# Performance work log

Measured on AMD Instinct MI355X. Metric: run time of the kernel, lower is better.

## Reference

```python
import jax, jax.numpy as jnp
import numpy as np

NUM_GRAPHS = 2048
NODES_PER_GRAPH = 256
N_NODES = NUM_GRAPHS * NODES_PER_GRAPH
N_EDGES = 2 * N_NODES
F_IN = 768
HID = 128
N_CLS = 2


def setup_inputs() -> dict:
    key = jax.random.key(0)
    ks = jax.random.split(key, 12)
    x = jax.random.normal(ks[0], (N_NODES, F_IN), dtype=jnp.float32)
    edge_index = jax.random.randint(ks[1], (2, N_EDGES), 0, N_NODES, dtype=jnp.int32)
    batch = jnp.repeat(jnp.arange(NUM_GRAPHS, dtype=jnp.int32), NODES_PER_GRAPH)
    s = 1.0 / np.sqrt(F_IN)
    sh = 1.0 / np.sqrt(HID)
    s2h = 1.0 / np.sqrt(2 * HID)
    return {
        "x": x,
        "edge_index": edge_index,
        "batch": batch,
        # SAGEConv: lin_l (aggregated neighbors, with bias) + lin_r (root, no bias)
        "W_l": jax.random.uniform(ks[2], (F_IN, HID), jnp.float32, -s, s),
        "b_l": jax.random.uniform(ks[3], (HID,), jnp.float32, -s, s),
        "W_r": jax.random.uniform(ks[4], (F_IN, HID), jnp.float32, -s, s),
        "W0": jax.random.uniform(ks[5], (F_IN, HID), jnp.float32, -s, s),
        "b0": jax.random.uniform(ks[6], (HID,), jnp.float32, -s, s),
        "W1": jax.random.uniform(ks[7], (2 * HID, HID), jnp.float32, -s2h, s2h),
        "b1": jax.random.uniform(ks[8], (HID,), jnp.float32, -s2h, s2h),
        "W2": jax.random.uniform(ks[9], (HID, N_CLS), jnp.float32, -sh, sh),
        "b2": jax.random.uniform(ks[10], (HID,), jnp.float32, -sh, sh)[:N_CLS],
    }


def reference(x, edge_index, batch, W_l, b_l, W_r, W0, b0, W1, b1, W2, b2):
    n = x.shape[0]
    src, dst = edge_index[0], edge_index[1]
    # SAGEConv with mean aggregation: gather -> segment mean -> transform
    msg_sum = jax.ops.segment_sum(x[src], dst, num_segments=n)      # [N, F]
    cnt = jax.ops.segment_sum(jnp.ones((src.shape[0],), x.dtype), dst, num_segments=n)
    agg = msg_sum / jnp.maximum(cnt, 1.0)[:, None]
    h = jax.nn.relu(agg @ W_l + b_l + x @ W_r)                       # [N, H]
    # global max pool per graph
    pooled = jax.ops.segment_max(h, batch, num_segments=NUM_GRAPHS)  # [G, H]
    # root (news) node = first node of each graph (batch is sorted)
    roots = jnp.searchsorted(batch, jnp.arange(NUM_GRAPHS, dtype=batch.dtype))
    news = jax.nn.relu(x[roots] @ W0 + b0)                           # [G, H]
    z = jax.nn.relu(jnp.concatenate([pooled, news], axis=1) @ W1 + b1)
    return jax.nn.log_softmax(z @ W2 + b2, axis=-1)                  # [G, 2]
```

## Files before the change

kernel.cpp:

```cpp
#include <hip/hip_runtime.h>

#define NGRAPH 2048
#define NPG 256
#define NNODE (NGRAPH*NPG)
#define NEDGE (2*NNODE)
#define FIN 768
#define HID 128
#define SLOTS 64
#define BK 32
#define NKT (FIN/BK)

typedef __bf16 bf16x8 __attribute__((ext_vector_type(8)));
typedef __bf16 bf16x4 __attribute__((ext_vector_type(4)));
typedef float f32x4 __attribute__((ext_vector_type(4)));

__device__ __forceinline__ float bflo(unsigned v) {
    return __uint_as_float((v & 0xffffu) << 16);
}
__device__ __forceinline__ float bfhi(unsigned v) {
    return __uint_as_float(v & 0xffff0000u);
}

__global__ __launch_bounds__(256) void k_prep(
    const float* __restrict__ Wl, const float* __restrict__ Wr,
    const float* __restrict__ W0, __bf16* __restrict__ WbT,
    int* __restrict__ deg)
{
    int idx = blockIdx.x * 256 + threadIdx.x;
    deg[idx] = 0;
    if (idx < 384 * FIN) {
        int n = idx / FIN;
        int k = idx - n * FIN;
        float v;
        if (n < HID)            v = Wl[k * HID + n];
        else if (n < 2 * HID)   v = Wr[k * HID + (n - HID)];
        else                    v = W0[k * HID + (n - 2 * HID)];
        WbT[idx] = (__bf16)v;
    }
}

template<int VMC, bool HASB, bool HASA, bool HASW>
__device__ __forceinline__ void gemm_tile(
    const char* rbuf, char* wbuf, int t, int lane, int wr, int wc,
    const float* asrc, const __bf16* WbT, int ktB, int ktA,
    f32x4& c0, f32x4& c1, f32x4& c2, f32x4& c3,
    f32x4& i0, f32x4& i1, f32x4& i2, f32x4& i3,
    int aoff0, int aoff1, f32x4 (&acc)[8][4])
{
    if constexpr (HASB) {
#pragma unroll
        for (int r = 0; r < 2; ++r) {
            int idx = r * 512 + t;
            int bn = idx >> 2, bj = idx & 3;
            int koff = (bj ^ ((bn >> 1) & 3)) << 3;
            const __bf16* g = WbT + bn * FIN + ktB * BK + koff;
            __builtin_amdgcn_global_load_lds(
                (__attribute__((address_space(1))) void*)g,
                (__attribute__((address_space(3))) void*)(wbuf + 16384 + idx * 16),
                16, 0, 0);
        }
        __builtin_amdgcn_sched_barrier(0);
    }
    if constexpr (HASA) {
        const f32x4* s4 = (const f32x4*)(asrc + ktA * BK);
        i0 = s4[0]; i1 = s4[1]; i2 = s4[2]; i3 = s4[3];
    }
    if constexpr (HASW) {
        bf16x8 h0, h1;
#pragma unroll
        for (int i = 0; i < 4; ++i) {
            h0[i]     = (__bf16)c0[i];
            h0[4 + i] = (__bf16)c1[i];
            h1[i]     = (__bf16)c2[i];
            h1[4 + i] = (__bf16)c3[i];
        }
        *(bf16x8*)(wbuf + aoff0) = h0;
        *(bf16x8*)(wbuf + aoff1) = h1;
    }
    const int kb = (lane >> 4) << 4;
    bf16x8 a[8], b[4];
#pragma unroll
    for (int m = 0; m < 8; ++m) {
        int row = wr * 128 + m * 16 + (lane & 15);
        a[m] = *(const bf16x8*)(rbuf + row * 64 + (kb ^ (((row >> 1) & 3) << 4)));
    }
#pragma unroll
    for (int n = 0; n < 4; ++n) {
        int row = wc * 64 + n * 16 + (lane & 15);
        b[n] = *(const bf16x8*)(rbuf + 16384 + row * 64 + (kb ^ (((row >> 1) & 3) << 4)));
    }
#pragma unroll
    for (int m = 0; m < 8; ++m)
#pragma unroll
        for (int n = 0; n < 4; ++n)
            acc[m][n] = __builtin_amdgcn_mfma_f32_16x16x32_bf16(
                a[m], b[n], acc[m][n], 0, 0, 0);
    if constexpr (VMC == 4) asm volatile("s_waitcnt vmcnt(4)" ::: "memory");
    else if constexpr (VMC == 0) asm volatile("s_waitcnt vmcnt(0)" ::: "memory");
    if constexpr (VMC >= 0) {
        asm volatile("s_waitcnt lgkmcnt(0)" ::: "memory");
        __builtin_amdgcn_s_barrier();
    }
}

__global__ __launch_bounds__(512, 1) void k_gemm(
    const float* __restrict__ X, const __bf16* __restrict__ WbT,
    __bf16* __restrict__ Yl, __bf16* __restrict__ Yr,
    const int* __restrict__ ei, int* __restrict__ deg, int* __restrict__ elist,
    const float* __restrict__ b0, float* __restrict__ news)
{
    __shared__ __align__(16) char sm[65536];
    const int t = threadIdx.x;
    const int lane = t & 63;
    const int w = t >> 6;

    if (blockIdx.x >= NNODE / 256) {
        const int wr = w >> 2;
        const int wc = w & 3;
        const int g0 = (blockIdx.x - NNODE / 256) * 64;

        f32x4 acc[2][2];
#pragma unroll
        for (int m = 0; m < 2; ++m)
#pragma unroll
            for (int n = 0; n < 2; ++n)
                acc[m][n] = (f32x4){0.f, 0.f, 0.f, 0.f};

        const int arow = t >> 3;
        const int ak = (t & 7) * 4;
        const float* asrc = X + (size_t)(g0 + arow) * (NPG * FIN) + ak;
        const int aoff = arow * 64 + (((ak * 2) ^ (((arow >> 1) & 3) << 4)));
        const __bf16* W0bT = WbT + (size_t)256 * FIN;

        for (int kt = 0; kt < NKT; ++kt) {
            const int k0 = kt * BK;
            __syncthreads();
            {
                f32x4 p = *(const f32x4*)(asrc + k0);
                bf16x4 h;
#pragma unroll
                for (int i = 0; i < 4; ++i) h[i] = (__bf16)p[i];
                *(bf16x4*)(sm + aoff) = h;
            }
            {
                int bn = t >> 2;
                int bj = t & 3;
                int koff = (bj ^ ((bn >> 1) & 3)) << 3;
                const __bf16* g = W0bT + bn * FIN + k0 + koff;
                __builtin_amdgcn_global_load_lds(
                    (__attribute__((address_space(1))) void*)g,
                    (__attribute__((address_space(3))) void*)(sm + 4096 + t * 16),
                    16, 0, 0);
            }
            __syncthreads();

            const int kb = (lane >> 4) << 4;
            bf16x8 a[2], b[2];
#pragma unroll
            for (int m = 0; m < 2; ++m) {
                int row = wr * 32 + m * 16 + (lane & 15);
                a[m] = *(const bf16x8*)(sm + row * 64 + (kb ^ (((row >> 1) & 3) << 4)));
            }
#pragma unroll
            for (int n = 0; n < 2; ++n) {
                int row = wc * 32 + n * 16 + (lane & 15);
                b[n] = *(const bf16x8*)(sm + 4096 + row * 64 + (kb ^ (((row >> 1) & 3) << 4)));
            }
#pragma unroll
            for (int m = 0; m < 2; ++m)
#pragma unroll
                for (int n = 0; n < 2; ++n)
                    acc[m][n] = __builtin_amdgcn_mfma_f32_16x16x32_bf16(
                        a[m], b[n], acc[m][n], 0, 0, 0);
        }

#pragma unroll
        for (int m = 0; m < 2; ++m) {
            const int rbase = wr * 32 + m * 16 + ((lane >> 4) << 2);
#pragma unroll
            for (int n = 0; n < 2; ++n) {
                const int col = wc * 32 + n * 16 + (lane & 15);
                const float bb = b0[col];
#pragma unroll
                for (int j = 0; j < 4; ++j)
                    news[(size_t)(g0 + rbase + j) * HID + col] =
                        fmaxf(acc[m][n][j] + bb, 0.f);
            }
        }
        return;
    }

    {
        int e = blockIdx.x * 512 + t;
        int src = ei[e];
        int dst = ei[NEDGE + e];
        int pos = atomicAdd(deg + dst, 1);
        if (pos < SLOTS) elist[(size_t)pos * NNODE + dst] = src;
    }
    asm volatile("s_waitcnt vmcnt(0)" ::: "memory");

    const int wr = w >> 2;
    const int wc = w & 3;
    const size_t node0 = (size_t)blockIdx.x * 256;

    f32x4 acc[8][4];
#pragma unroll
    for (int m = 0; m < 8; ++m)
#pragma unroll
        for (int n = 0; n < 4; ++n)
            acc[m][n] = (f32x4){0.f, 0.f, 0.f, 0.f};

    const int arow = t >> 1;
    const int ak = (t & 1) * 16;
    const float* asrc = X + (node0 + arow) * FIN + ak;
    const int axr = ((arow >> 1) & 3) << 4;
    const int aoff0 = arow * 64 + ((ak * 2) ^ axr);
    const int aoff1 = arow * 64 + ((ak * 2 + 16) ^ axr);

    char* buf0 = sm;
    char* buf1 = sm + 32768;
    f32x4 qa0, qa1, qa2, qa3;
    f32x4 qb0, qb1, qb2, qb3;

    {
#pragma unroll
        for (int r = 0; r < 2; ++r) {
            int idx = r * 512 + t;
            int bn = idx >> 2, bj = idx & 3;
            int koff = (bj ^ ((bn >> 1) & 3)) << 3;
            const __bf16* g = WbT + bn * FIN + 0 * BK + koff;
            __builtin_amdgcn_global_load_lds(
                (__attribute__((address_space(1))) void*)g,
                (__attribute__((address_space(3))) void*)(buf0 + 16384 + idx * 16),
                16, 0, 0);
        }
        __builtin_amdgcn_sched_barrier(0);
        {
            const f32x4* s4 = (const f32x4*)(asrc);
            qa0 = s4[0]; qa1 = s4[1]; qa2 = s4[2]; qa3 = s4[3];
        }
        {
            const f32x4* s4 = (const f32x4*)(asrc + 1 * BK);
            qb0 = s4[0]; qb1 = s4[1]; qb2 = s4[2]; qb3 = s4[3];
        }
        bf16x8 h0, h1;
#pragma unroll
        for (int i = 0; i < 4; ++i) {
            h0[i]     = (__bf16)qa0[i];
            h0[4 + i] = (__bf16)qa1[i];
            h1[i]     = (__bf16)qa2[i];
            h1[4 + i] = (__bf16)qa3[i];
        }
        *(bf16x8*)(buf0 + aoff0) = h0;
        *(bf16x8*)(buf0 + aoff1) = h1;
        asm volatile("s_waitcnt vmcnt(4)" ::: "memory");
        asm volatile("s_waitcnt lgkmcnt(0)" ::: "memory");
        __builtin_amdgcn_s_barrier();
    }

    for (int kt = 0; kt < 22; kt += 2) {
        gemm_tile<4, true, true, true>(buf0, buf1, t, lane, wr, wc, asrc, WbT,
            kt + 1, kt + 2, qb0, qb1, qb2, qb3, qa0, qa1, qa2, qa3,
            aoff0, aoff1, acc);
        gemm_tile<4, true, true, true>(buf1, buf0, t, lane, wr, wc, asrc, WbT,
            kt + 2, kt + 3, qa0, qa1, qa2, qa3, qb0, qb1, qb2, qb3,
            aoff0, aoff1, acc);
    }
    gemm_tile<0, true, false, true>(buf0, buf1, t, lane, wr, wc, asrc, WbT,
        23, 0, qb0, qb1, qb2, qb3, qa0, qa1, qa2, qa3, aoff0, aoff1, acc);
    gemm_tile<-1, false, false, false>(buf1, buf0, t, lane, wr, wc, asrc, WbT,
        0, 0, qa0, qa1, qa2, qa3, qb0, qb1, qb2, qb3, aoff0, aoff1, acc);

#pragma unroll
    for (int m = 0; m < 8; ++m) {
        const int rbase = wr * 128 + m * 16 + ((lane >> 4) << 2);
#pragma unroll
        for (int n = 0; n < 4; ++n) {
            const int col = wc * 64 + n * 16 + (lane & 15);
            __bf16* dst = (col < HID) ? Yl : Yr;
            const int c = col & (HID - 1);
#pragma unroll
            for (int j = 0; j < 4; ++j)
                dst[(node0 + rbase + j) * HID + c] = (__bf16)acc[m][n][j];
        }
    }
}

__global__ __launch_bounds__(512) void k_fused(
    const int* __restrict__ deg, const int* __restrict__ elist,
    const __bf16* __restrict__ Yl, const __bf16* __restrict__ Yr,
    const float* __restrict__ bl, const float* __restrict__ news,
    const float* __restrict__ W1, const float* __restrict__ b1,
    const float* __restrict__ W2, const float* __restrict__ b2,
    float* __restrict__ out)
{
    __shared__ int   sdeg[NPG];
    __shared__ int   sel[4 * NPG];
    __shared__ float red[8 * HID];
    __shared__ float cat[2 * HID];
    __shared__ float zs[HID];

    const int g = blockIdx.x;
    const int t = threadIdx.x;
    const size_t gbase = (size_t)g * NPG;

    if (t < NPG) sdeg[t] = deg[gbase + t];
#pragma unroll
    for (int r = 0; r < 2; ++r) {
        int idx = r * 512 + t;
        sel[idx] = elist[(size_t)(idx >> 8) * NNODE + gbase + (idx & 255)];
    }
    __syncthreads();

    const int l = t & 63;
    const int sub = t >> 6;
    const int half = l >> 5;
    const int lj = l & 31;
    const int d4 = lj * 4;
    const float4 blv = *(const float4*)(bl + d4);
    const uint2* yl2 = (const uint2*)Yl;
    const uint2* yr2 = (const uint2*)Yr;

    float m0 = -3.0e38f, m1 = -3.0e38f, m2 = -3.0e38f, m3 = -3.0e38f;

    for (int k4 = 0; k4 < 8; ++k4) {
        const int nA = sub + 8 * (4 * k4 + half);
        const int nB = sub + 8 * (4 * k4 + 2 + half);
        const int dgA = sdeg[nA], dgB = sdeg[nB];
        int sA[4], sB[4];
#pragma unroll
        for (int j = 0; j < 4; ++j) {
            int cA = sel[j * NPG + nA];
            int cB = sel[j * NPG + nB];
            sA[j] = (j < dgA) ? cA : 0;
            sB[j] = (j < dgB) ? cB : 0;
        }
        uint2 vA[4], vB[4];
#pragma unroll
        for (int j = 0; j < 4; ++j) {
            vA[j] = yl2[(size_t)sA[j] * 32 + lj];
            vB[j] = yl2[(size_t)sB[j] * 32 + lj];
        }
        const uint2 yA = yr2[(gbase + nA) * 32 + lj];
        const uint2 yB = yr2[(gbase + nB) * 32 + lj];

        float s0A = 0.f, s1A = 0.f, s2A = 0.f, s3A = 0.f;
        float s0B = 0.f, s1B = 0.f, s2B = 0.f, s3B = 0.f;
#pragma unroll
        for (int j = 0; j < 4; ++j) {
            const float mA = (j < dgA) ? 1.f : 0.f;
            const float mB = (j < dgB) ? 1.f : 0.f;
            s0A = fmaf(mA, bflo(vA[j].x), s0A);
            s1A = fmaf(mA, bfhi(vA[j].x), s1A);
            s2A = fmaf(mA, bflo(vA[j].y), s2A);
            s3A = fmaf(mA, bfhi(vA[j].y), s3A);
            s0B = fmaf(mB, bflo(vB[j].x), s0B);
            s1B = fmaf(mB, bfhi(vB[j].x), s1B);
            s2B = fmaf(mB, bflo(vB[j].y), s2B);
            s3B = fmaf(mB, bfhi(vB[j].y), s3B);
        }
        int mx = dgA > dgB ? dgA : dgB;
        mx = max(mx, __shfl_xor(mx, 32));
        mx = mx < SLOTS ? mx : SLOTS;
        for (int j = 4; j < mx; ++j) {
            int cA = elist[(size_t)j * NNODE + gbase + nA];
            int cB = elist[(size_t)j * NNODE + gbase + nB];
            int eA = (j < dgA) ? cA : 0;
            int eB = (j < dgB) ? cB : 0;
            uint2 wA = yl2[(size_t)eA * 32 + lj];
            uint2 wB = yl2[(size_t)eB * 32 + lj];
            const float mA = (j < dgA) ? 1.f : 0.f;
            const float mB = (j < dgB) ? 1.f : 0.f;
            s0A = fmaf(mA, bflo(wA.x), s0A);
            s1A = fmaf(mA, bfhi(wA.x), s1A);
            s2A = fmaf(mA, bflo(wA.y), s2A);
            s3A = fmaf(mA, bfhi(wA.y), s3A);
            s0B = fmaf(mB, bflo(wB.x), s0B);
            s1B = fmaf(mB, bfhi(wB.x), s1B);
            s2B = fmaf(mB, bflo(wB.y), s2B);
            s3B = fmaf(mB, bfhi(wB.y), s3B);
        }
        const float invA = 1.f / fmaxf((float)dgA, 1.f);
        const float invB = 1.f / fmaxf((float)dgB, 1.f);
        float h0 = fmaf(s0A, invA, blv.x) + bflo(yA.x);
        float h1 = fmaf(s1A, invA, blv.y) + bfhi(yA.x);
        float h2 = fmaf(s2A, invA, blv.z) + bflo(yA.y);
        float h3 = fmaf(s3A, invA, blv.w) + bfhi(yA.y);
        m0 = fmaxf(m0, fmaxf(h0, 0.f));
        m1 = fmaxf(m1, fmaxf(h1, 0.f));
        m2 = fmaxf(m2, fmaxf(h2, 0.f));
        m3 = fmaxf(m3, fmaxf(h3, 0.f));
        h0 = fmaf(s0B, invB, blv.x) + bflo(yB.x);
        h1 = fmaf(s1B, invB, blv.y) + bfhi(yB.x);
        h2 = fmaf(s2B, invB, blv.z) + bflo(yB.y);
        h3 = fmaf(s3B, invB, blv.w) + bfhi(yB.y);
        m0 = fmaxf(m0, fmaxf(h0, 0.f));
        m1 = fmaxf(m1, fmaxf(h1, 0.f));
        m2 = fmaxf(m2, fmaxf(h2, 0.f));
        m3 = fmaxf(m3, fmaxf(h3, 0.f));
    }
    m0 = fmaxf(m0, __shfl_xor(m0, 32));
    m1 = fmaxf(m1, __shfl_xor(m1, 32));
    m2 = fmaxf(m2, __shfl_xor(m2, 32));
    m3 = fmaxf(m3, __shfl_xor(m3, 32));
    if (half == 0) {
        float4 mv = {m0, m1, m2, m3};
        *(float4*)(red + sub * HID + d4) = mv;
    }
    __syncthreads();

    if (t < HID) {
        float v = red[t];
#pragma unroll
        for (int s = 1; s < 8; ++s) v = fmaxf(v, red[s * HID + t]);
        cat[t] = v;
        cat[HID + t] = news[(size_t)g * HID + t];
    }
    __syncthreads();

    if (t < HID) {
        float a0 = 0.f, a1 = 0.f, a2 = 0.f, a3 = 0.f;
        for (int k = 0; k < 2 * HID; k += 4) {
            a0 = fmaf(cat[k + 0], W1[(k + 0) * HID + t], a0);
            a1 = fmaf(cat[k + 1], W1[(k + 1) * HID + t], a1);
            a2 = fmaf(cat[k + 2], W1[(k + 2) * HID + t], a2);
            a3 = fmaf(cat[k + 3], W1[(k + 3) * HID + t], a3);
        }
        zs[t] = fmaxf((a0 + a1) + (a2 + a3) + b1[t], 0.f);
    }
    __syncthreads();

    if (t < 64) {
        float z0 = zs[t * 2], z1 = zs[t * 2 + 1];
        float p0 = fmaf(z0, W2[t * 4 + 0], z1 * W2[t * 4 + 2]);
        float p1 = fmaf(z0, W2[t * 4 + 1], z1 * W2[t * 4 + 3]);
#pragma unroll
        for (int off = 32; off; off >>= 1) {
            p0 += __shfl_down(p0, off);
            p1 += __shfl_down(p1, off);
        }
        if (t == 0) {
            float l0 = p0 + b2[0], l1 = p1 + b2[1];
            float mx = fmaxf(l0, l1);
            float lse = mx + logf(expf(l0 - mx) + expf(l1 - mx));
            out[(size_t)g * 2 + 0] = l0 - lse;
            out[(size_t)g * 2 + 1] = l1 - lse;
        }
    }
}

extern "C" void kernel_launch(void* const* d_in, const int* in_sizes, int n_in,
                              void* d_out, int out_size, void* d_ws, size_t ws_size,
                              hipStream_t stream)
{
    const float* x   = (const float*)d_in[0];
    const int*   ei  = (const int*)d_in[1];
    const float* W_l = (const float*)d_in[3];
    const float* b_l = (const float*)d_in[4];
    const float* W_r = (const float*)d_in[5];
    const float* W0  = (const float*)d_in[6];
    const float* b0  = (const float*)d_in[7];
    const float* W1  = (const float*)d_in[8];
    const float* b1  = (const float*)d_in[9];
    const float* W2  = (const float*)d_in[10];
    const float* b2  = (const float*)d_in[11];
    float* out = (float*)d_out;

    char* ws = (char*)d_ws;
    size_t off = 0;
    auto alloc = [&](size_t bytes) {
        char* p = ws + off;
        off += (bytes + 511) & ~(size_t)511;
        return p;
    };
    __bf16* WbT   = (__bf16*)alloc((size_t)384 * FIN * 2);
    __bf16* Yl    = (__bf16*)alloc((size_t)NNODE * HID * 2);
    __bf16* Yr    = (__bf16*)alloc((size_t)NNODE * HID * 2);
    int*    deg   = (int*)alloc((size_t)NNODE * 4);
    int*    elist = (int*)alloc((size_t)NNODE * SLOTS * 4);
    float*  news  = (float*)alloc((size_t)NGRAPH * HID * 4);
    if (off > ws_size) return;

    k_prep<<<NNODE / 256, 256, 0, stream>>>(W_l, W_r, W0, WbT, deg);
    k_gemm<<<NNODE / 256 + NGRAPH / 64, 512, 0, stream>>>(
        x, WbT, Yl, Yr, ei, deg, elist, b0, news);
    k_fused<<<NGRAPH, 512, 0, stream>>>(deg, elist, Yl, Yr, b_l, news,
                                        W1, b1, W2, b2, out);
}
```

Measured before the change: 593.0 us.

## Triple-buffer LDS tiles in the node GEMM to deepen the load pipeline

Moves the main GEMM loop from double to triple LDS buffering. The weight tile is prefetched two K-steps ahead via global_load_lds while activations are staged one step ahead in registers. The explicit vmcnt waits are removed, relying on in-order completion implied by the compiler's waits on the register A-loads. The kernel now uses 96KB of dynamic shared memory. This aims to hide global-load latency behind MFMA work, but risks a race on the async LDS writes and launch issues from the larger LDS request.

New measurement: 600.2 us. No clear change (+1.2%).

```diff
diff --git a/kernel.cpp b/kernel.cpp
--- a/kernel.cpp
+++ b/kernel.cpp
@@ -39,10 +39,10 @@
     }
 }
 
-template<int VMC, bool HASB, bool HASA, bool HASW>
-__device__ __forceinline__ void gemm_tile(
-    const char* rbuf, char* wbuf, int t, int lane, int wr, int wc,
-    const float* asrc, const __bf16* WbT, int ktB, int ktA,
+template<bool HASB, bool HASA, bool HASW, bool BAR>
+__device__ __forceinline__ void tile3(
+    const char* rbuf, char* wbufN, char* wbufS, int t, int lane, int wr, int wc,
+    const float* asrc, const __bf16* WbT, int ktS,
     f32x4& c0, f32x4& c1, f32x4& c2, f32x4& c3,
     f32x4& i0, f32x4& i1, f32x4& i2, f32x4& i3,
     int aoff0, int aoff1, f32x4 (&acc)[8][4])
@@ -53,16 +53,16 @@
             int idx = r * 512 + t;
             int bn = idx >> 2, bj = idx & 3;
             int koff = (bj ^ ((bn >> 1) & 3)) << 3;
-            const __bf16* g = WbT + bn * FIN + ktB * BK + koff;
+            const __bf16* g = WbT + bn * FIN + ktS * BK + koff;
             __builtin_amdgcn_global_load_lds(
                 (__attribute__((address_space(1))) void*)g,
-                (__attribute__((address_space(3))) void*)(wbuf + 16384 + idx * 16),
+                (__attribute__((address_space(3))) void*)(wbufS + 16384 + idx * 16),
                 16, 0, 0);
         }
         __builtin_amdgcn_sched_barrier(0);
     }
     if constexpr (HASA) {
-        const f32x4* s4 = (const f32x4*)(asrc + ktA * BK);
+        const f32x4* s4 = (const f32x4*)(asrc + ktS * BK);
         i0 = s4[0]; i1 = s4[1]; i2 = s4[2]; i3 = s4[3];
     }
     if constexpr (HASW) {
@@ -74,8 +74,8 @@
             h1[i]     = (__bf16)c2[i];
             h1[4 + i] = (__bf16)c3[i];
         }
-        *(bf16x8*)(wbuf + aoff0) = h0;
-        *(bf16x8*)(wbuf + aoff1) = h1;
+        *(bf16x8*)(wbufN + aoff0) = h0;
+        *(bf16x8*)(wbufN + aoff1) = h1;
     }
     const int kb = (lane >> 4) << 4;
     bf16x8 a[8], b[4];
@@ -95,9 +95,7 @@
         for (int n = 0; n < 4; ++n)
             acc[m][n] = __builtin_amdgcn_mfma_f32_16x16x32_bf16(
                 a[m], b[n], acc[m][n], 0, 0, 0);
-    if constexpr (VMC == 4) asm volatile("s_waitcnt vmcnt(4)" ::: "memory");
-    else if constexpr (VMC == 0) asm volatile("s_waitcnt vmcnt(0)" ::: "memory");
-    if constexpr (VMC >= 0) {
+    if constexpr (BAR) {
         asm volatile("s_waitcnt lgkmcnt(0)" ::: "memory");
         __builtin_amdgcn_s_barrier();
     }
@@ -109,7 +107,7 @@
     const int* __restrict__ ei, int* __restrict__ deg, int* __restrict__ elist,
     const float* __restrict__ b0, float* __restrict__ news)
 {
-    __shared__ __align__(16) char sm[65536];
+    extern __shared__ __align__(16) char sm[];
     const int t = threadIdx.x;
     const int lane = t & 63;
     const int w = t >> 6;
@@ -219,6 +217,7 @@
 
     char* buf0 = sm;
     char* buf1 = sm + 32768;
+    char* buf2 = sm + 65536;
     f32x4 qa0, qa1, qa2, qa3;
     f32x4 qb0, qb1, qb2, qb3;
 
@@ -239,6 +238,18 @@
             const f32x4* s4 = (const f32x4*)(asrc);
             qa0 = s4[0]; qa1 = s4[1]; qa2 = s4[2]; qa3 = s4[3];
         }
+#pragma unroll
+        for (int r = 0; r < 2; ++r) {
+            int idx = r * 512 + t;
+            int bn = idx >> 2, bj = idx & 3;
+            int koff = (bj ^ ((bn >> 1) & 3)) << 3;
+            const __bf16* g = WbT + bn * FIN + 1 * BK + koff;
+            __builtin_amdgcn_global_load_lds(
+                (__attribute__((address_space(1))) void*)g,
+                (__attribute__((address_space(3))) void*)(buf1 + 16384 + idx * 16),
+                16, 0, 0);
+        }
+        __builtin_amdgcn_sched_barrier(0);
         {
             const f32x4* s4 = (const f32x4*)(asrc + 1 * BK);
             qb0 = s4[0]; qb1 = s4[1]; qb2 = s4[2]; qb3 = s4[3];
@@ -253,23 +264,36 @@
         }
         *(bf16x8*)(buf0 + aoff0) = h0;
         *(bf16x8*)(buf0 + aoff1) = h1;
-        asm volatile("s_waitcnt vmcnt(4)" ::: "memory");
         asm volatile("s_waitcnt lgkmcnt(0)" ::: "memory");
         __builtin_amdgcn_s_barrier();
     }
 
-    for (int kt = 0; kt < 22; kt += 2) {
-        gemm_tile<4, true, true, true>(buf0, buf1, t, lane, wr, wc, asrc, WbT,
-            kt + 1, kt + 2, qb0, qb1, qb2, qb3, qa0, qa1, qa2, qa3,
-            aoff0, aoff1, acc);
-        gemm_tile<4, true, true, true>(buf1, buf0, t, lane, wr, wc, asrc, WbT,
-            kt + 2, kt + 3, qa0, qa1, qa2, qa3, qb0, qb1, qb2, qb3,
-            aoff0, aoff1, acc);
-    }
-    gemm_tile<0, true, false, true>(buf0, buf1, t, lane, wr, wc, asrc, WbT,
-        23, 0, qb0, qb1, qb2, qb3, qa0, qa1, qa2, qa3, aoff0, aoff1, acc);
-    gemm_tile<-1, false, false, false>(buf1, buf0, t, lane, wr, wc, asrc, WbT,
-        0, 0, qa0, qa1, qa2, qa3, qb0, qb1, qb2, qb3, aoff0, aoff1, acc);
+    for (int base = 0; base < 18; base += 6) {
+        tile3<1,1,1,1>(buf0, buf1, buf2, t, lane, wr, wc, asrc, WbT, base + 2,
+                       qb0, qb1, qb2, qb3, qa0, qa1, qa2, qa3, aoff0, aoff1, acc);
+        tile3<1,1,1,1>(buf1, buf2, buf0, t, lane, wr, wc, asrc, WbT, base + 3,
+                       qa0, qa1, qa2, qa3, qb0, qb1, qb2, qb3, aoff0, aoff1, acc);
+        tile3<1,1,1,1>(buf2, buf0, buf1, t, lane, wr, wc, asrc, WbT, base + 4,
+                       qb0, qb1, qb2, qb3, qa0, qa1, qa2, qa3, aoff0, aoff1, acc);
+        tile3<1,1,1,1>(buf0, buf1, buf2, t, lane, wr, wc, asrc, WbT, base + 5,
+                       qa0, qa1, qa2, qa3, qb0, qb1, qb2, qb3, aoff0, aoff1, acc);
+        tile3<1,1,1,1>(buf1, buf2, buf0, t, lane, wr, wc, asrc, WbT, base + 6,
+                       qb0, qb1, qb2, qb3, qa0, qa1, qa2, qa3, aoff0, aoff1, acc);
+        tile3<1,1,1,1>(buf2, buf0, buf1, t, lane, wr, wc, asrc, WbT, base + 7,
+                       qa0, qa1, qa2, qa3, qb0, qb1, qb2, qb3, aoff0, aoff1, acc);
+    }
+    tile3<1,1,1,1>(buf0, buf1, buf2, t, lane, wr, wc, asrc, WbT, 20,
+                   qb0, qb1, qb2, qb3, qa0, qa1, qa2, qa3, aoff0, aoff1, acc);
+    tile3<1,1,1,1>(buf1, buf2, buf0, t, lane, wr, wc, asrc, WbT, 21,
+                   qa0, qa1, qa2, qa3, qb0, qb1, qb2, qb3, aoff0, aoff1, acc);
+    tile3<1,1,1,1>(buf2, buf0, buf1, t, lane, wr, wc, asrc, WbT, 22,
+                   qb0, qb1, qb2, qb3, qa0, qa1, qa2, qa3, aoff0, aoff1, acc);
+    tile3<1,1,1,1>(buf0, buf1, buf2, t, lane, wr, wc, asrc, WbT, 23,
+                   qa0, qa1, qa2, qa3, qb0, qb1, qb2, qb3, aoff0, aoff1, acc);
+    tile3<0,0,1,1>(buf1, buf2, buf0, t, lane, wr, wc, asrc, WbT, 0,
+                   qb0, qb1, qb2, qb3, qa0, qa1, qa2, qa3, aoff0, aoff1, acc);
+    tile3<0,0,0,0>(buf2, buf0, buf1, t, lane, wr, wc, asrc, WbT, 0,
+                   qa0, qa1, qa2, qa3, qb0, qb1, qb2, qb3, aoff0, aoff1, acc);
 
 #pragma unroll
     for (int m = 0; m < 8; ++m) {
@@ -482,7 +506,7 @@
     if (off > ws_size) return;
 
     k_prep<<<NNODE / 256, 256, 0, stream>>>(W_l, W_r, W0, WbT, deg);
-    k_gemm<<<NNODE / 256 + NGRAPH / 64, 512, 0, stream>>>(
+    k_gemm<<<NNODE / 256 + NGRAPH / 64, 512, 98304, stream>>>(
         x, WbT, Yl, Yr, ei, deg, elist, b0, news);
     k_fused<<<NGRAPH, 512, 0, stream>>>(deg, elist, Yl, Yr, b_l, news,
                                         W1, b1, W2, b2, out);
```

## Load X A-tiles as contiguous 256B pairs per thread across two K-tiles

Applied to the files above, without the earlier changes.

Reworks how the X (fp32) operand is fetched in the main GEMM: each thread now loads 32 contiguous floats covering two K-tiles (one half of a 64-wide span) every other iteration, and threads alternate which half converts and writes to LDS. This gives longer contiguous per-thread reads and fewer load issue points, with a reshuffled vmcnt schedule (wait 8 / wait 0 alternating). It costs more registers (two 8-vector sets) and leaves half the threads idle during each conversion step, which may unbalance work.

New measurement: 663.9 us. +12.0%, slower.

```diff
diff --git a/kernel.cpp b/kernel.cpp
--- a/kernel.cpp
+++ b/kernel.cpp
@@ -13,6 +13,9 @@
 typedef __bf16 bf16x8 __attribute__((ext_vector_type(8)));
 typedef __bf16 bf16x4 __attribute__((ext_vector_type(4)));
 typedef float f32x4 __attribute__((ext_vector_type(4)));
+
+#define AS1 __attribute__((address_space(1)))
+#define AS3 __attribute__((address_space(3)))
 
 __device__ __forceinline__ float bflo(unsigned v) {
     return __uint_as_float((v & 0xffffu) << 16);
@@ -39,13 +42,12 @@
     }
 }
 
-template<int VMC, bool HASB, bool HASA, bool HASW>
-__device__ __forceinline__ void gemm_tile(
+template<int VMC, bool HASB, bool HASPAIR, bool HASCVT, int CVTHALF>
+__device__ __forceinline__ void tileP(
     const char* rbuf, char* wbuf, int t, int lane, int wr, int wc,
-    const float* asrc, const __bf16* WbT, int ktB, int ktA,
-    f32x4& c0, f32x4& c1, f32x4& c2, f32x4& c3,
-    f32x4& i0, f32x4& i1, f32x4& i2, f32x4& i3,
-    int aoff0, int aoff1, f32x4 (&acc)[8][4])
+    const float* apair, const __bf16* WbT, int ktB, int pairIdx,
+    f32x4 (&ql)[8], f32x4 (&qc)[8],
+    int arow, int axr, int half, f32x4 (&acc)[8][4])
 {
     if constexpr (HASB) {
 #pragma unroll
@@ -55,27 +57,29 @@
             int koff = (bj ^ ((bn >> 1) & 3)) << 3;
             const __bf16* g = WbT + bn * FIN + ktB * BK + koff;
             __builtin_amdgcn_global_load_lds(
-                (__attribute__((address_space(1))) void*)g,
-                (__attribute__((address_space(3))) void*)(wbuf + 16384 + idx * 16),
-                16, 0, 0);
+                (AS1 void*)g, (AS3 void*)(wbuf + 16384 + idx * 16), 16, 0, 0);
         }
         __builtin_amdgcn_sched_barrier(0);
     }
-    if constexpr (HASA) {
-        const f32x4* s4 = (const f32x4*)(asrc + ktA * BK);
-        i0 = s4[0]; i1 = s4[1]; i2 = s4[2]; i3 = s4[3];
-    }
-    if constexpr (HASW) {
-        bf16x8 h0, h1;
-#pragma unroll
-        for (int i = 0; i < 4; ++i) {
-            h0[i]     = (__bf16)c0[i];
-            h0[4 + i] = (__bf16)c1[i];
-            h1[i]     = (__bf16)c2[i];
-            h1[4 + i] = (__bf16)c3[i];
-        }
-        *(bf16x8*)(wbuf + aoff0) = h0;
-        *(bf16x8*)(wbuf + aoff1) = h1;
+    if constexpr (HASPAIR) {
+        const f32x4* s4 = (const f32x4*)(apair + pairIdx * 64);
+#pragma unroll
+        for (int i = 0; i < 8; ++i) ql[i] = s4[i];
+        __builtin_amdgcn_sched_barrier(0);
+    }
+    if constexpr (HASCVT) {
+        if (half == CVTHALF) {
+#pragma unroll
+            for (int s = 0; s < 4; ++s) {
+                bf16x8 h;
+#pragma unroll
+                for (int i = 0; i < 4; ++i) {
+                    h[i]     = (__bf16)qc[2 * s][i];
+                    h[4 + i] = (__bf16)qc[2 * s + 1][i];
+                }
+                *(bf16x8*)(wbuf + arow * 64 + ((s * 16) ^ axr)) = h;
+            }
+        }
     }
     const int kb = (lane >> 4) << 4;
     bf16x8 a[8], b[4];
@@ -95,7 +99,7 @@
         for (int n = 0; n < 4; ++n)
             acc[m][n] = __builtin_amdgcn_mfma_f32_16x16x32_bf16(
                 a[m], b[n], acc[m][n], 0, 0, 0);
-    if constexpr (VMC == 4) asm volatile("s_waitcnt vmcnt(4)" ::: "memory");
+    if constexpr (VMC == 8) asm volatile("s_waitcnt vmcnt(8)" ::: "memory");
     else if constexpr (VMC == 0) asm volatile("s_waitcnt vmcnt(0)" ::: "memory");
     if constexpr (VMC >= 0) {
         asm volatile("s_waitcnt lgkmcnt(0)" ::: "memory");
@@ -148,9 +152,7 @@
                 int koff = (bj ^ ((bn >> 1) & 3)) << 3;
                 const __bf16* g = W0bT + bn * FIN + k0 + koff;
                 __builtin_amdgcn_global_load_lds(
-                    (__attribute__((address_space(1))) void*)g,
-                    (__attribute__((address_space(3))) void*)(sm + 4096 + t * 16),
-                    16, 0, 0);
+                    (AS1 void*)g, (AS3 void*)(sm + 4096 + t * 16), 16, 0, 0);
             }
             __syncthreads();
 
@@ -211,16 +213,13 @@
             acc[m][n] = (f32x4){0.f, 0.f, 0.f, 0.f};
 
     const int arow = t >> 1;
-    const int ak = (t & 1) * 16;
-    const float* asrc = X + (node0 + arow) * FIN + ak;
+    const int half = t & 1;
     const int axr = ((arow >> 1) & 3) << 4;
-    const int aoff0 = arow * 64 + ((ak * 2) ^ axr);
-    const int aoff1 = arow * 64 + ((ak * 2 + 16) ^ axr);
+    const float* apair = X + (node0 + arow) * FIN + half * 32;
 
     char* buf0 = sm;
     char* buf1 = sm + 32768;
-    f32x4 qa0, qa1, qa2, qa3;
-    f32x4 qb0, qb1, qb2, qb3;
+    f32x4 set0[8], set1[8];
 
     {
 #pragma unroll
@@ -230,46 +229,49 @@
             int koff = (bj ^ ((bn >> 1) & 3)) << 3;
             const __bf16* g = WbT + bn * FIN + 0 * BK + koff;
             __builtin_amdgcn_global_load_lds(
-                (__attribute__((address_space(1))) void*)g,
-                (__attribute__((address_space(3))) void*)(buf0 + 16384 + idx * 16),
-                16, 0, 0);
+                (AS1 void*)g, (AS3 void*)(buf0 + 16384 + idx * 16), 16, 0, 0);
         }
         __builtin_amdgcn_sched_barrier(0);
         {
-            const f32x4* s4 = (const f32x4*)(asrc);
-            qa0 = s4[0]; qa1 = s4[1]; qa2 = s4[2]; qa3 = s4[3];
-        }
-        {
-            const f32x4* s4 = (const f32x4*)(asrc + 1 * BK);
-            qb0 = s4[0]; qb1 = s4[1]; qb2 = s4[2]; qb3 = s4[3];
-        }
-        bf16x8 h0, h1;
-#pragma unroll
-        for (int i = 0; i < 4; ++i) {
-            h0[i]     = (__bf16)qa0[i];
-            h0[4 + i] = (__bf16)qa1[i];
-            h1[i]     = (__bf16)qa2[i];
-            h1[4 + i] = (__bf16)qa3[i];
-        }
-        *(bf16x8*)(buf0 + aoff0) = h0;
-        *(bf16x8*)(buf0 + aoff1) = h1;
-        asm volatile("s_waitcnt vmcnt(4)" ::: "memory");
+            const f32x4* s4 = (const f32x4*)(apair);
+#pragma unroll
+            for (int i = 0; i < 8; ++i) set0[i] = s4[i];
+        }
+        if (half == 0) {
+#pragma unroll
+            for (int s = 0; s < 4; ++s) {
+                bf16x8 h;
+#pragma unroll
+                for (int i = 0; i < 4; ++i) {
+                    h[i]     = (__bf16)set0[2 * s][i];
+                    h[4 + i] = (__bf16)set0[2 * s + 1][i];
+                }
+                *(bf16x8*)(buf0 + arow * 64 + ((s * 16) ^ axr)) = h;
+            }
+        }
+        asm volatile("s_waitcnt vmcnt(0)" ::: "memory");
         asm volatile("s_waitcnt lgkmcnt(0)" ::: "memory");
         __builtin_amdgcn_s_barrier();
     }
 
-    for (int kt = 0; kt < 22; kt += 2) {
-        gemm_tile<4, true, true, true>(buf0, buf1, t, lane, wr, wc, asrc, WbT,
-            kt + 1, kt + 2, qb0, qb1, qb2, qb3, qa0, qa1, qa2, qa3,
-            aoff0, aoff1, acc);
-        gemm_tile<4, true, true, true>(buf1, buf0, t, lane, wr, wc, asrc, WbT,
-            kt + 2, kt + 3, qa0, qa1, qa2, qa3, qb0, qb1, qb2, qb3,
-            aoff0, aoff1, acc);
-    }
-    gemm_tile<0, true, false, true>(buf0, buf1, t, lane, wr, wc, asrc, WbT,
-        23, 0, qb0, qb1, qb2, qb3, qa0, qa1, qa2, qa3, aoff0, aoff1, acc);
-    gemm_tile<-1, false, false, false>(buf1, buf0, t, lane, wr, wc, asrc, WbT,
-        0, 0, qa0, qa1, qa2, qa3, qb0, qb1, qb2, qb3, aoff0, aoff1, acc);
+    for (int p = 0; p < 10; p += 2) {
+        tileP<8, 1, 1, 1, 1>(buf0, buf1, t, lane, wr, wc, apair, WbT,
+                             2 * p + 1, p + 1, set1, set0, arow, axr, half, acc);
+        tileP<0, 1, 0, 1, 0>(buf1, buf0, t, lane, wr, wc, apair, WbT,
+                             2 * p + 2, 0, set1, set1, arow, axr, half, acc);
+        tileP<8, 1, 1, 1, 1>(buf0, buf1, t, lane, wr, wc, apair, WbT,
+                             2 * p + 3, p + 2, set0, set1, arow, axr, half, acc);
+        tileP<0, 1, 0, 1, 0>(buf1, buf0, t, lane, wr, wc, apair, WbT,
+                             2 * p + 4, 0, set0, set0, arow, axr, half, acc);
+    }
+    tileP<8, 1, 1, 1, 1>(buf0, buf1, t, lane, wr, wc, apair, WbT,
+                         21, 11, set1, set0, arow, axr, half, acc);
+    tileP<0, 1, 0, 1, 0>(buf1, buf0, t, lane, wr, wc, apair, WbT,
+                         22, 0, set1, set1, arow, axr, half, acc);
+    tileP<0, 1, 0, 1, 1>(buf0, buf1, t, lane, wr, wc, apair, WbT,
+                         23, 0, set0, set1, arow, axr, half, acc);
+    tileP<-1, 0, 0, 0, 0>(buf1, buf0, t, lane, wr, wc, apair, WbT,
+                          0, 0, set0, set0, arow, axr, half, acc);
 
 #pragma unroll
     for (int m = 0; m < 8; ++m) {
```
